# Optimization experiments

Hardware: AMD Instinct MI355X
Metric: run time of the kernel (lower is better)

Reference implementation:

```python
import jax, jax.numpy as jnp
import numpy as np

B, T, C, HS = 8, 2048, 1024, 64

def setup_inputs() -> dict:
    key = jax.random.key(0)
    ks = jax.random.split(key, 6)
    return {
        "q_vec": jax.random.normal(ks[0], (B, T, C), dtype=jnp.float32),
        "k_vec": jax.random.normal(ks[1], (B, T, C), dtype=jnp.float32),
        "v_vec": jax.random.normal(ks[2], (B, T, C), dtype=jnp.float32),
        "mask": jnp.ones((B, T), dtype=jnp.int32),
        "Wq": jax.random.normal(ks[3], (C, HS), dtype=jnp.float32) * (C ** -0.5),
        "Wk": jax.random.normal(ks[4], (C, HS), dtype=jnp.float32) * (C ** -0.5),
        "Wv": jax.random.normal(ks[5], (C, HS), dtype=jnp.float32) * (C ** -0.5),
    }

def reference(q_vec, k_vec, v_vec, mask, Wq, Wk, Wv):
    # bias-free linear projections: [B,T,C] @ [C,HS] -> [B,T,HS]
    q = jnp.einsum('btc,ch->bth', q_vec, Wq)
    k = jnp.einsum('btc,ch->bth', k_vec, Wk)
    v = jnp.einsum('btc,ch->bth', v_vec, Wv)
    scale = k.shape[-1] ** -0.5
    # full T x T score matrix, as in the original module
    scores = jnp.einsum('bth,bsh->bts', q, k) * scale  # [B,T,T]
    Tq = scores.shape[1]
    # _expand_along_time: expanded[b,i,j] = mask[b,j], then causal tril
    mask_exp = jnp.broadcast_to(mask[:, None, :].astype(jnp.float32), scores.shape)
    tril = jnp.tril(jnp.ones((Tq, Tq), dtype=jnp.float32))
    combined = mask_exp * tril[None, :, :]
    scores = jnp.where(combined == 0, -jnp.inf, scores)
    attn = jax.nn.softmax(scores, axis=-1)
    # dropout p=0.0 (eval) -> identity
    out = jnp.einsum('bts,bsh->bth', attn, v)  # [B,T,HS]
    return out
```

## Files before the change

### kernel.cpp

```cpp
#include <hip/hip_runtime.h>
#include <hip/hip_bf16.h>
#include <cmath>
#include <stdint.h>

#define B_ 8
#define T_ 2048
#define C_ 1024
#define HS_ 64
#define NS 8
#define LP 72

typedef __attribute__((ext_vector_type(8))) short short8;
typedef __attribute__((ext_vector_type(4))) float floatx4;

__device__ inline unsigned short f2bf(float f) {
    union { float f; unsigned u; } v; v.f = f;
    unsigned r = v.u + 0x7FFF + ((v.u >> 16) & 1);
    return (unsigned short)(r >> 16);
}
__device__ inline unsigned pk2bf(float a, float b) {
    union { __hip_bfloat162 h; unsigned u; } v;
    v.h = __float22bfloat162_rn(float2{a, b});
    return v.u;
}
__device__ inline float bf2f(unsigned short u) {
    union { unsigned u; float f; } w; w.u = ((unsigned)u) << 16; return w.f;
}

__global__ __launch_bounds__(256) void prep_wt(const float* __restrict__ Wq,
                                               const float* __restrict__ Wk,
                                               const float* __restrict__ Wv,
                                               unsigned short* __restrict__ wf) {
    int p   = blockIdx.x >> 4;
    int blk = blockIdx.x & 15;
    const float* W = (p == 0) ? Wq : (p == 1) ? Wk : Wv;
    unsigned short* Wf = wf + p * 65536;
    #pragma unroll
    for (int u2 = 0; u2 < 2; ++u2) {
        int u = blk * 512 + u2 * 256 + threadIdx.x;
        int lane = u & 63;
        int nt = (u >> 6) & 3;
        int ks = u >> 8;
        int l16 = lane & 15, quad = lane >> 4;
        int col  = nt * 16 + l16;
        int krow = ks * 32 + quad * 8;
        union { short8 s; unsigned short h[8]; } o;
        #pragma unroll
        for (int j = 0; j < 8; ++j)
            o.h[j] = f2bf(W[(krow + j) * 64 + col]);
        *(short8*)(Wf + (long)u * 8) = o.s;
    }
}

__global__ __launch_bounds__(256, 4) void proj_kernel(
    const float* __restrict__ qv, const float* __restrict__ kv, const float* __restrict__ vv,
    const unsigned short* __restrict__ wf,
    unsigned short* __restrict__ qb, unsigned short* __restrict__ kb, unsigned short* __restrict__ vb)
{
    const int tid  = threadIdx.x;
    const int wave = tid >> 6, lane = tid & 63, quad = lane >> 4, l16 = lane & 15;
    const int wid  = blockIdx.x * 4 + wave;
    const int p    = wid >> 10;
    const int tile = wid & 1023;

    const float* X = (p == 0) ? qv : (p == 1) ? kv : vv;
    unsigned short* Ob = (p == 0) ? qb : (p == 1) ? kb : vb;
    const unsigned short* Wf = wf + p * 65536;
    const float oscale = (p == 0) ? 0.125f : 1.0f;

    const float* xp = X + ((long)tile * 16 + l16) * C_ + quad * 8;
    const unsigned short* wp = Wf + lane * 8;

    floatx4 acc[4] = { {0,0,0,0},{0,0,0,0},{0,0,0,0},{0,0,0,0} };

    floatx4 xq[4][2];
    short8  wq[2][4];
    #pragma unroll
    for (int i = 0; i < 4; ++i) {
        xq[i][0] = *(const floatx4*)(xp + i * 32);
        xq[i][1] = *(const floatx4*)(xp + i * 32 + 4);
    }
    #pragma unroll
    for (int i = 0; i < 2; ++i)
        #pragma unroll
        for (int nt = 0; nt < 4; ++nt)
            wq[i][nt] = *(const short8*)(wp + (i * 4 + nt) * 512);

    #pragma unroll
    for (int ks = 0; ks < 32; ++ks) {
        const int xc = ks & 3, wc = ks & 1;
        floatx4 ca = xq[xc][0], cb = xq[xc][1];
        short8 b0 = wq[wc][0], b1 = wq[wc][1], b2 = wq[wc][2], b3 = wq[wc][3];

        if (ks + 4 < 32) {
            xq[xc][0] = *(const floatx4*)(xp + (ks + 4) * 32);
            xq[xc][1] = *(const floatx4*)(xp + (ks + 4) * 32 + 4);
        }
        if (ks + 2 < 32) {
            #pragma unroll
            for (int nt = 0; nt < 4; ++nt)
                wq[wc][nt] = *(const short8*)(wp + ((ks + 2) * 4 + nt) * 512);
        }

        union { short8 s; unsigned u[4]; } af;
        af.u[0] = pk2bf(ca[0], ca[1]);
        af.u[1] = pk2bf(ca[2], ca[3]);
        af.u[2] = pk2bf(cb[0], cb[1]);
        af.u[3] = pk2bf(cb[2], cb[3]);

        acc[0] = __builtin_amdgcn_mfma_f32_16x16x32_bf16(af.s, b0, acc[0], 0, 0, 0);
        acc[1] = __builtin_amdgcn_mfma_f32_16x16x32_bf16(af.s, b1, acc[1], 0, 0, 0);
        acc[2] = __builtin_amdgcn_mfma_f32_16x16x32_bf16(af.s, b2, acc[2], 0, 0, 0);
        acc[3] = __builtin_amdgcn_mfma_f32_16x16x32_bf16(af.s, b3, acc[3], 0, 0, 0);
    }

    unsigned short* op = Ob + ((long)tile * 16 + quad * 4) * HS_ + l16;
    #pragma unroll
    for (int nt = 0; nt < 4; ++nt)
        #pragma unroll
        for (int r = 0; r < 4; ++r)
            op[r * HS_ + nt * 16] = f2bf(acc[nt][r] * oscale);
}

__global__ __launch_bounds__(256) void attn_partial(
    const unsigned short* __restrict__ qb, const unsigned short* __restrict__ kb,
    const unsigned short* __restrict__ vb, const int* __restrict__ mask,
    unsigned short* __restrict__ Opart, float* __restrict__ Mpart, float* __restrict__ Lpart)
{
    const int s  = blockIdx.x & (NS - 1);
    const int bq = blockIdx.x >> 3;
    const int qt = bq & 31;
    const int b  = bq >> 5;
    if (s > qt) return;

    __shared__ unsigned short Klds[64 * LP];
    __shared__ unsigned short Vt[64 * LP];
    __shared__ unsigned short Plds[4][16 * LP];

    const int tid = threadIdx.x;
    const int wave = tid >> 6, lane = tid & 63, quad = lane >> 4, l16 = lane & 15;

    const int qrow = qt * 64 + wave * 16 + l16;
    const unsigned short* qp = qb + ((long)(b * T_ + qrow)) * HS_;
    short8 aq0 = *(const short8*)&qp[0  + quad * 8];
    short8 aq1 = *(const short8*)&qp[32 + quad * 8];

    floatx4 acc_o[4] = { {0,0,0,0},{0,0,0,0},{0,0,0,0},{0,0,0,0} };
    float m_r[4] = { -INFINITY, -INFINITY, -INFINITY, -INFINITY };
    float l_r[4] = { 0.f, 0.f, 0.f, 0.f };

    const int rowg = qt * 64 + wave * 16 + quad * 4;

    const int skey = tid >> 3;
    const int sf8  = (tid & 7) * 8;
    const int vp = tid & 31, vg = tid >> 5;

    for (int c = s; c <= qt; c += NS) {
        const int kc = c * 64;
        #pragma unroll
        for (int it = 0; it < 2; ++it) {
            int key = it * 32 + skey;
            *(short8*)&Klds[key * LP + sf8] =
                *(const short8*)&kb[((long)(b * T_ + kc + key)) * HS_ + sf8];
        }
        {
            const unsigned short* v0p = &vb[((long)(b * T_ + kc + 2 * vp)) * HS_ + vg * 8];
            short8 v0 = *(const short8*)v0p;
            short8 v1 = *(const short8*)(v0p + HS_);
            #pragma unroll
            for (int j = 0; j < 8; ++j) {
                unsigned pr = (unsigned)(unsigned short)v0[j] |
                              ((unsigned)(unsigned short)v1[j] << 16);
                *(unsigned*)&Vt[(vg * 8 + j) * LP + 2 * vp] = pr;
            }
        }
        __syncthreads();

        floatx4 sv[4];
        #pragma unroll
        for (int kt = 0; kt < 4; ++kt) {
            floatx4 a = {0.f, 0.f, 0.f, 0.f};
            short8 bk0 = *(short8*)&Klds[(kt * 16 + l16) * LP + 0  + quad * 8];
            short8 bk1 = *(short8*)&Klds[(kt * 16 + l16) * LP + 32 + quad * 8];
            a = __builtin_amdgcn_mfma_f32_16x16x32_bf16(aq0, bk0, a, 0, 0, 0);
            a = __builtin_amdgcn_mfma_f32_16x16x32_bf16(aq1, bk1, a, 0, 0, 0);
            sv[kt] = a;
        }

        const bool lastc = (c == qt);
        #pragma unroll
        for (int kt = 0; kt < 4; ++kt) {
            int key = kc + kt * 16 + l16;
            int mk = mask[b * T_ + key];
            #pragma unroll
            for (int r = 0; r < 4; ++r) {
                bool dead = (mk == 0) || (lastc && key > rowg + r);
                if (dead) sv[kt][r] = -INFINITY;
            }
        }

        float alpha[4];
        #pragma unroll
        for (int r = 0; r < 4; ++r) {
            float mx = fmaxf(fmaxf(sv[0][r], sv[1][r]), fmaxf(sv[2][r], sv[3][r]));
            #pragma unroll
            for (int off = 1; off < 16; off <<= 1)
                mx = fmaxf(mx, __shfl_xor(mx, off));
            float mn = fmaxf(m_r[r], mx);
            float a_ = __expf(m_r[r] - mn);
            float ps = 0.f;
            #pragma unroll
            for (int kt = 0; kt < 4; ++kt) {
                float pv = __expf(sv[kt][r] - mn);
                sv[kt][r] = pv;
                ps += pv;
            }
            #pragma unroll
            for (int off = 1; off < 16; off <<= 1)
                ps += __shfl_xor(ps, off);
            l_r[r] = l_r[r] * a_ + ps;
            m_r[r] = mn;
            alpha[r] = a_;
        }
        #pragma unroll
        for (int nt = 0; nt < 4; ++nt)
            #pragma unroll
            for (int r = 0; r < 4; ++r)
                acc_o[nt][r] *= alpha[r];

        unsigned short* pl = Plds[wave];
        #pragma unroll
        for (int kt = 0; kt < 4; ++kt)
            #pragma unroll
            for (int r = 0; r < 4; ++r)
                pl[(quad * 4 + r) * LP + kt * 16 + l16] = f2bf(sv[kt][r]);
        short8 ap0 = *(short8*)&pl[l16 * LP + 0  + quad * 8];
        short8 ap1 = *(short8*)&pl[l16 * LP + 32 + quad * 8];

        #pragma unroll
        for (int nt = 0; nt < 4; ++nt) {
            short8 bv0 = *(short8*)&Vt[(nt * 16 + l16) * LP + 0  + quad * 8];
            short8 bv1 = *(short8*)&Vt[(nt * 16 + l16) * LP + 32 + quad * 8];
            acc_o[nt] = __builtin_amdgcn_mfma_f32_16x16x32_bf16(ap0, bv0, acc_o[nt], 0, 0, 0);
            acc_o[nt] = __builtin_amdgcn_mfma_f32_16x16x32_bf16(ap1, bv1, acc_o[nt], 0, 0, 0);
        }
        __syncthreads();
    }

    unsigned short* Op = Opart + (long)blockIdx.x * 4096;
    #pragma unroll
    for (int nt = 0; nt < 4; ++nt)
        #pragma unroll
        for (int r = 0; r < 4; ++r)
            Op[(wave * 16 + quad * 4 + r) * 64 + nt * 16 + l16] = f2bf(acc_o[nt][r]);
    if (l16 == 0) {
        #pragma unroll
        for (int r = 0; r < 4; ++r) {
            int rl = wave * 16 + quad * 4 + r;
            Mpart[(long)blockIdx.x * 64 + rl] = m_r[r];
            Lpart[(long)blockIdx.x * 64 + rl] = l_r[r];
        }
    }
}

__global__ __launch_bounds__(256) void attn_combine(
    const unsigned short* __restrict__ Opart, const float* __restrict__ Mpart,
    const float* __restrict__ Lpart, float* __restrict__ out)
{
    const int half = blockIdx.x & 1;
    const int bq = blockIdx.x >> 1;
    const int qt = bq & 31;
    const int b  = bq >> 5;
    const int nsp = (qt + 1 < NS) ? qt + 1 : NS;

    const int row  = (threadIdx.x >> 3) + half * 32;
    const int colg = (threadIdx.x & 7) * 8;
    const long base = (long)bq * NS;

    float M = -INFINITY;
    #pragma unroll
    for (int sp = 0; sp < NS; ++sp)
        if (sp < nsp) M = fmaxf(M, Mpart[(base + sp) * 64 + row]);

    float w[NS];
    float L = 0.f;
    #pragma unroll
    for (int sp = 0; sp < NS; ++sp)
        if (sp < nsp) {
            float e = __expf(Mpart[(base + sp) * 64 + row] - M);
            w[sp] = e;
            L += e * Lpart[(base + sp) * 64 + row];
        }

    float acc[8] = {0,0,0,0,0,0,0,0};
    #pragma unroll
    for (int sp = 0; sp < NS; ++sp)
        if (sp < nsp) {
            const unsigned short* Op = Opart + (base + sp) * 4096 + row * 64 + colg;
            short8 o = *(const short8*)Op;
            float ws = w[sp];
            #pragma unroll
            for (int j = 0; j < 8; ++j)
                acc[j] += ws * bf2f((unsigned short)o[j]);
        }

    float inv = 1.0f / L;
    float* op = out + ((long)(b * T_ + qt * 64 + row)) * HS_ + colg;
    floatx4 o0 = { acc[0] * inv, acc[1] * inv, acc[2] * inv, acc[3] * inv };
    floatx4 o1 = { acc[4] * inv, acc[5] * inv, acc[6] * inv, acc[7] * inv };
    *(floatx4*)op = o0;
    *(floatx4*)(op + 4) = o1;
}

extern "C" void kernel_launch(void* const* d_in, const int* in_sizes, int n_in,
                              void* d_out, int out_size, void* d_ws, size_t ws_size,
                              hipStream_t stream)
{
    const float* qv = (const float*)d_in[0];
    const float* kv = (const float*)d_in[1];
    const float* vv = (const float*)d_in[2];
    const int*   mask = (const int*)d_in[3];
    const float* Wq = (const float*)d_in[4];
    const float* Wk = (const float*)d_in[5];
    const float* Wv = (const float*)d_in[6];
    float* out = (float*)d_out;

    unsigned short* wf    = (unsigned short*)d_ws;
    unsigned short* qbuf  = wf + 3 * C_ * HS_;
    unsigned short* kbuf  = qbuf + (long)B_ * T_ * HS_;
    unsigned short* vbuf  = kbuf + (long)B_ * T_ * HS_;
    unsigned short* Opart = vbuf + (long)B_ * T_ * HS_;
    float* Mpart = (float*)(Opart + (long)B_ * 32 * NS * 4096);
    float* Lpart = Mpart + (long)B_ * 32 * NS * 64;

    prep_wt<<<48, 256, 0, stream>>>(Wq, Wk, Wv, wf);
    proj_kernel<<<768, 256, 0, stream>>>(qv, kv, vv, wf, qbuf, kbuf, vbuf);
    attn_partial<<<B_ * 32 * NS, 256, 0, stream>>>(qbuf, kbuf, vbuf, mask, Opart, Mpart, Lpart);
    attn_combine<<<B_ * 32 * 2, 256, 0, stream>>>(Opart, Mpart, Lpart, out);
}
```

Before: 264.9 us.

## Split projection K-dimension across four waves with LDS reduction

The projection kernel now assigns one 16-row tile per block and splits the 1024-long reduction across four waves, each covering 256 columns. Partial accumulators are summed through shared memory before wave 0 writes bf16 output. This gives four times as many blocks and shorter per-wave dependency chains, so more memory-level parallelism is available for streaming the fp32 inputs. The cost is an LDS reduction plus a barrier, with three of four waves idle during the write-out. prep_wt is also rewritten to read W coalesced and scatter its bf16 writes.

New measurement: 252.1 us. 1.05x faster.

```diff
diff --git a/kernel.cpp b/kernel.cpp
--- a/kernel.cpp
+++ b/kernel.cpp
@@ -36,90 +36,98 @@
     const float* W = (p == 0) ? Wq : (p == 1) ? Wk : Wv;
     unsigned short* Wf = wf + p * 65536;
     #pragma unroll
-    for (int u2 = 0; u2 < 2; ++u2) {
-        int u = blk * 512 + u2 * 256 + threadIdx.x;
-        int lane = u & 63;
-        int nt = (u >> 6) & 3;
-        int ks = u >> 8;
-        int l16 = lane & 15, quad = lane >> 4;
-        int col  = nt * 16 + l16;
-        int krow = ks * 32 + quad * 8;
-        union { short8 s; unsigned short h[8]; } o;
-        #pragma unroll
-        for (int j = 0; j < 8; ++j)
-            o.h[j] = f2bf(W[(krow + j) * 64 + col]);
-        *(short8*)(Wf + (long)u * 8) = o.s;
-    }
-}
-
-__global__ __launch_bounds__(256, 4) void proj_kernel(
+    for (int it = 0; it < 16; ++it) {
+        int idx = blk * 4096 + it * 256 + threadIdx.x;
+        int k = idx >> 6, col = idx & 63;
+        int ks = k >> 5, quad = (k >> 3) & 3, j = k & 7;
+        int nt = col >> 4, l16 = col & 15;
+        Wf[(ks * 256 + nt * 64 + quad * 16 + l16) * 8 + j] = f2bf(W[idx]);
+    }
+}
+
+__global__ __launch_bounds__(256, 6) void proj_kernel(
     const float* __restrict__ qv, const float* __restrict__ kv, const float* __restrict__ vv,
     const unsigned short* __restrict__ wf,
     unsigned short* __restrict__ qb, unsigned short* __restrict__ kb, unsigned short* __restrict__ vb)
 {
+    __shared__ float rlds[3][16][68];
+
     const int tid  = threadIdx.x;
     const int wave = tid >> 6, lane = tid & 63, quad = lane >> 4, l16 = lane & 15;
-    const int wid  = blockIdx.x * 4 + wave;
-    const int p    = wid >> 10;
-    const int tile = wid & 1023;
+    const int p    = blockIdx.x >> 10;
+    const int tile = blockIdx.x & 1023;
 
     const float* X = (p == 0) ? qv : (p == 1) ? kv : vv;
     unsigned short* Ob = (p == 0) ? qb : (p == 1) ? kb : vb;
     const unsigned short* Wf = wf + p * 65536;
     const float oscale = (p == 0) ? 0.125f : 1.0f;
 
-    const float* xp = X + ((long)tile * 16 + l16) * C_ + quad * 8;
-    const unsigned short* wp = Wf + lane * 8;
+    const float* xp = X + ((long)tile * 16 + l16) * C_ + wave * 256 + quad * 8;
+    const unsigned short* wp = Wf + (wave * 8) * 4 * 512 + lane * 8;
 
     floatx4 acc[4] = { {0,0,0,0},{0,0,0,0},{0,0,0,0},{0,0,0,0} };
 
-    floatx4 xq[4][2];
+    floatx4 xq[2][2];
     short8  wq[2][4];
-    #pragma unroll
-    for (int i = 0; i < 4; ++i) {
-        xq[i][0] = *(const floatx4*)(xp + i * 32);
-        xq[i][1] = *(const floatx4*)(xp + i * 32 + 4);
-    }
-    #pragma unroll
-    for (int i = 0; i < 2; ++i)
-        #pragma unroll
-        for (int nt = 0; nt < 4; ++nt)
-            wq[i][nt] = *(const short8*)(wp + (i * 4 + nt) * 512);
-
-    #pragma unroll
-    for (int ks = 0; ks < 32; ++ks) {
-        const int xc = ks & 3, wc = ks & 1;
-        floatx4 ca = xq[xc][0], cb = xq[xc][1];
-        short8 b0 = wq[wc][0], b1 = wq[wc][1], b2 = wq[wc][2], b3 = wq[wc][3];
-
-        if (ks + 4 < 32) {
-            xq[xc][0] = *(const floatx4*)(xp + (ks + 4) * 32);
-            xq[xc][1] = *(const floatx4*)(xp + (ks + 4) * 32 + 4);
-        }
-        if (ks + 2 < 32) {
+    xq[0][0] = *(const floatx4*)(xp);
+    xq[0][1] = *(const floatx4*)(xp + 4);
+    xq[1][0] = *(const floatx4*)(xp + 32);
+    xq[1][1] = *(const floatx4*)(xp + 36);
+    #pragma unroll
+    for (int nt = 0; nt < 4; ++nt) wq[0][nt] = *(const short8*)(wp + nt * 512);
+    #pragma unroll
+    for (int nt = 0; nt < 4; ++nt) wq[1][nt] = *(const short8*)(wp + (4 + nt) * 512);
+
+    #pragma unroll
+    for (int s = 0; s < 8; ++s) {
+        const int bi = s & 1;
+        floatx4 ca = xq[bi][0], cb = xq[bi][1];
+        short8 b0 = wq[bi][0], b1 = wq[bi][1], b2 = wq[bi][2], b3 = wq[bi][3];
+
+        if (s + 2 < 8) {
+            xq[bi][0] = *(const floatx4*)(xp + (s + 2) * 32);
+            xq[bi][1] = *(const floatx4*)(xp + (s + 2) * 32 + 4);
             #pragma unroll
             for (int nt = 0; nt < 4; ++nt)
-                wq[wc][nt] = *(const short8*)(wp + ((ks + 2) * 4 + nt) * 512);
-        }
-
-        union { short8 s; unsigned u[4]; } af;
+                wq[bi][nt] = *(const short8*)(wp + ((s + 2) * 4 + nt) * 512);
+        }
+
+        union { short8 s8; unsigned u[4]; } af;
         af.u[0] = pk2bf(ca[0], ca[1]);
         af.u[1] = pk2bf(ca[2], ca[3]);
         af.u[2] = pk2bf(cb[0], cb[1]);
         af.u[3] = pk2bf(cb[2], cb[3]);
 
-        acc[0] = __builtin_amdgcn_mfma_f32_16x16x32_bf16(af.s, b0, acc[0], 0, 0, 0);
-        acc[1] = __builtin_amdgcn_mfma_f32_16x16x32_bf16(af.s, b1, acc[1], 0, 0, 0);
-        acc[2] = __builtin_amdgcn_mfma_f32_16x16x32_bf16(af.s, b2, acc[2], 0, 0, 0);
-        acc[3] = __builtin_amdgcn_mfma_f32_16x16x32_bf16(af.s, b3, acc[3], 0, 0, 0);
-    }
-
-    unsigned short* op = Ob + ((long)tile * 16 + quad * 4) * HS_ + l16;
-    #pragma unroll
-    for (int nt = 0; nt < 4; ++nt)
-        #pragma unroll
-        for (int r = 0; r < 4; ++r)
-            op[r * HS_ + nt * 16] = f2bf(acc[nt][r] * oscale);
+        acc[0] = __builtin_amdgcn_mfma_f32_16x16x32_bf16(af.s8, b0, acc[0], 0, 0, 0);
+        acc[1] = __builtin_amdgcn_mfma_f32_16x16x32_bf16(af.s8, b1, acc[1], 0, 0, 0);
+        acc[2] = __builtin_amdgcn_mfma_f32_16x16x32_bf16(af.s8, b2, acc[2], 0, 0, 0);
+        acc[3] = __builtin_amdgcn_mfma_f32_16x16x32_bf16(af.s8, b3, acc[3], 0, 0, 0);
+    }
+
+    if (wave) {
+        #pragma unroll
+        for (int nt = 0; nt < 4; ++nt)
+            #pragma unroll
+            for (int r = 0; r < 4; ++r)
+                rlds[wave - 1][quad * 4 + r][nt * 16 + l16] = acc[nt][r];
+    }
+    __syncthreads();
+    if (wave == 0) {
+        #pragma unroll
+        for (int nt = 0; nt < 4; ++nt)
+            #pragma unroll
+            for (int r = 0; r < 4; ++r)
+                acc[nt][r] += rlds[0][quad * 4 + r][nt * 16 + l16]
+                            + rlds[1][quad * 4 + r][nt * 16 + l16]
+                            + rlds[2][quad * 4 + r][nt * 16 + l16];
+
+        unsigned short* op = Ob + ((long)tile * 16 + quad * 4) * HS_ + l16;
+        #pragma unroll
+        for (int nt = 0; nt < 4; ++nt)
+            #pragma unroll
+            for (int r = 0; r < 4; ++r)
+                op[r * HS_ + nt * 16] = f2bf(acc[nt][r] * oscale);
+    }
 }
 
 __global__ __launch_bounds__(256) void attn_partial(
@@ -334,7 +342,7 @@
     float* Lpart = Mpart + (long)B_ * 32 * NS * 64;
 
     prep_wt<<<48, 256, 0, stream>>>(Wq, Wk, Wv, wf);
-    proj_kernel<<<768, 256, 0, stream>>>(qv, kv, vv, wf, qbuf, kbuf, vbuf);
+    proj_kernel<<<3072, 256, 0, stream>>>(qv, kv, vv, wf, qbuf, kbuf, vbuf);
     attn_partial<<<B_ * 32 * NS, 256, 0, stream>>>(qbuf, kbuf, vbuf, mask, Opart, Mpart, Lpart);
     attn_combine<<<B_ * 32 * 2, 256, 0, stream>>>(Opart, Mpart, Lpart, out);
 }
```
